# Kernel tuning notes

Hardware: AMD Instinct MI355X
Metric: run time of the kernel (lower is better)

Reference implementation:

```python
import jax, jax.numpy as jnp
import numpy as np

B, N, F, H, K = 4, 512, 64, 64, 64
EPS = 1e-14


def _pair_proj(h, W):
    # Linear over concat([h_j, h_i]) == h_j @ W[:F] + h_i @ W[F:], broadcast to [B,N,N,out]
    f = h.shape[-1]
    pj = h @ W[:f]   # [B,N,out] contribution of h.unsqueeze(-3) (index j)
    pi = h @ W[f:]   # [B,N,out] contribution of h.unsqueeze(-2) (index i)
    return pj[:, None, :, :] + pi[:, :, None, :]


def setup_inputs() -> dict:
    key = jax.random.key(0)
    ks = jax.random.split(key, 10)
    def w(k, shape, fan_in):
        return (jax.random.normal(k, shape, dtype=jnp.float32) / np.float32(np.sqrt(fan_in)))
    return {
        "h": jax.random.normal(ks[0], (B, N, F), dtype=jnp.float32),
        "x": jax.random.normal(ks[1], (B, N, 3), dtype=jnp.float32),
        "W_ew": w(ks[2], (2 * F, K), 2 * F), "b_ew": jnp.zeros((K,), jnp.float32),
        "W_sa": w(ks[3], (2 * F, 1), 2 * F),
        "W_es": w(ks[4], (2 * F + 1, H), 2 * F + 1), "b_es": jnp.zeros((H,), jnp.float32),
        "W_c1": w(ks[5], (H, H), H), "b_c1": jnp.zeros((H,), jnp.float32),
        "W_c2": w(ks[6], (H, 1), H), "b_c2": jnp.zeros((1,), jnp.float32),
        "W_n": w(ks[7], (F + H + K, H), F + H + K), "b_n": jnp.zeros((H,), jnp.float32),
    }


def reference(h, x, W_ew, b_ew, W_sa, W_es, b_es, W_c1, b_c1, W_c2, b_c2, W_n, b_n):
    # x_minus_xt[b,i,j] = x[b,j] - x[b,i]    [B,N,N,3]
    xmx = x[:, None, :, :] - x[:, :, None, :]
    norm = jnp.sqrt(jax.nn.relu(jnp.sum(xmx * xmx, axis=-1, keepdims=True)) + EPS)  # [B,N,N,1]
    spatial_att = jax.nn.softmax(norm, axis=-2)                                    # softmax over j
    filtered = 1.0 / (norm + 0.1)                                                  # [B,N,N,1]

    # edge_weight_mlp: tanh(Linear(2F -> K)) over h_cat_ht, without materializing the concat
    ew = jnp.tanh(_pair_proj(h, W_ew) + b_ew)                                      # [B,N,N,K]
    # semantic_attention_mlp: LeakyReLU(Linear(2F -> 1, no bias))
    sem_att = jax.nn.leaky_relu(_pair_proj(h, W_sa), negative_slope=0.01)          # [B,N,N,1]

    # x_minus_xt_att_sum = sum_j ew[b,i,j,k] * (xmx / norm^2)[b,i,j,c] -> [B,N,K,3]
    v = xmx / (norm * norm + EPS)
    att_sum = jnp.einsum('bijk,bijc->bikc', ew, v)
    att_norm = jnp.sqrt(jax.nn.relu(jnp.sum(att_sum * att_sum, axis=-1)) + EPS)    # [B,N,K]

    # edge_summary_mlp: SiLU(Linear(cat([filtered, h_j, h_i]) -> H))
    pre = filtered * W_es[0] + _pair_proj(h, W_es[1:]) + b_es                      # [B,N,N,H]
    h_e = jax.nn.silu(pre)

    # coordinate update: Linear->SiLU->Linear(H->1)
    coord = jax.nn.silu(h_e @ W_c1 + b_c1) @ W_c2 + b_c2                           # [B,N,N,1]
    x_new = jnp.sum(xmx * coord, axis=-2) + x                                      # sum over j

    h_e_agg = jnp.sum(sem_att * spatial_att * h_e, axis=-2)                        # [B,N,H]
    h_new = jnp.concatenate([h, h_e_agg, att_norm], axis=-1) @ W_n + b_n           # [B,N,H]
    return h_new, x_new
```

## Files before the change

kernel.cpp:

```cpp
#include <hip/hip_runtime.h>

#define B_ 4
#define N_ 512
#define F_ 64
#define H_ 64
#define K_ 64
#define BN_ (B_*N_)
#define EPS_ 1e-14f
#define TSC 2.8853900817779268f

typedef __attribute__((ext_vector_type(8))) short short8;
typedef __attribute__((ext_vector_type(4))) float f32x4;
typedef __attribute__((ext_vector_type(2))) float f32x2;

__device__ __forceinline__ unsigned short f2bf(float f) {
    const unsigned u = __float_as_uint(f);
    return (unsigned short)((u + 0x7FFFu + ((u >> 16) & 1u)) >> 16);
}
__device__ __forceinline__ unsigned short cvt_bf16(float f) {
    unsigned r;
    asm("v_cvt_pk_bf16_f32 %0, %1, %1" : "=v"(r) : "v"(f));
    return (unsigned short)r;
}
__device__ __forceinline__ unsigned cvt_pk_bf16(float lo, float hi) {
    unsigned r;
    asm("v_cvt_pk_bf16_f32 %0, %1, %2" : "=v"(r) : "v"(lo), "v"(hi));
    return r;
}
__device__ __forceinline__ float exp2_raw(float x) {
    float r;
    asm("v_exp_f32 %0, %1" : "=v"(r) : "v"(x));
    return r;
}
__device__ __forceinline__ float lane_bcast(float v, int lane) {
    return __int_as_float(__builtin_amdgcn_readlane(__float_as_int(v), lane));
}
__device__ __forceinline__ float rcpf(float x) { return __builtin_amdgcn_rcpf(x); }
__device__ __forceinline__ float fast_silu(float x) {
    return x * rcpf(1.0f + __expf(-x));
}

#define W_PJ2  0
#define W_PIEW (BN_*128)
#define W_PIES (BN_*128 + BN_*64)
#define W_PJSA (BN_*128 + 2*BN_*64)
#define W_PISA (BN_*128 + 2*BN_*64 + BN_)

__global__ __launch_bounds__(64) void proj_kernel(
    const float* __restrict__ h, const float* __restrict__ W_ew,
    const float* __restrict__ W_sa, const float* __restrict__ W_es,
    float* __restrict__ ws)
{
    const int node = blockIdx.x;
    const int t = threadIdx.x;
    __shared__ float sh[F_];
    sh[t] = h[node*F_ + t];
    __syncthreads();
    float a_jew=0.f, a_iew=0.f, a_jes=0.f, a_ies=0.f, a_jsa=0.f, a_isa=0.f;
    #pragma unroll 8
    for (int f = 0; f < F_; ++f) {
        const float hv = sh[f];
        a_jew += hv * W_ew[f*K_ + t];
        a_iew += hv * W_ew[(F_+f)*K_ + t];
        a_jes += hv * W_es[(1+f)*H_ + t];
        a_ies += hv * W_es[(1+F_+f)*H_ + t];
        a_jsa += hv * W_sa[f];
        a_isa += hv * W_sa[F_+f];
    }
    ws[W_PJ2 + (size_t)node*128 + t*2 + 0] = a_jew * TSC;
    ws[W_PJ2 + (size_t)node*128 + t*2 + 1] = a_jes;
    ws[W_PIEW + node*K_ + t] = a_iew;
    ws[W_PIES + node*H_ + t] = a_ies;
    if (t == 0) { ws[W_PJSA + node] = a_jsa; ws[W_PISA + node] = a_isa; }
}

__global__ __launch_bounds__(256, 6) void main_kernel(
    const float* __restrict__ h, const float* __restrict__ x,
    const float* __restrict__ b_ew, const float* __restrict__ b_es,
    const float* __restrict__ W_es, const float* __restrict__ W_c1,
    const float* __restrict__ b_c1, const float* __restrict__ W_c2,
    const float* __restrict__ b_c2, const float* __restrict__ W_n,
    const float* __restrict__ b_n,
    const float* __restrict__ ws, float* __restrict__ out)
{
    const int bi   = blockIdx.x;
    const int b    = bi >> 9;
    const int base = b * N_;
    const int tid  = threadIdx.x;
    const int w    = tid >> 6;
    const int lane = tid & 63;
    const int quad = lane >> 4;
    const int l16  = lane & 15;

    __shared__ unsigned short he_buf[4][16][72];
    __shared__ float sdA[4][64][4];
    __shared__ float coord_buf[4][64];
    __shared__ unsigned short WT[64*64];
    __shared__ float s_bw[64][2];

    float* const epi = (float*)&he_buf[0][0][0];
#define S_ATT(cmp, wv, ln) epi[(cmp)*256 + (wv)*64 + (ln)]
#define S_HEA(wv, ln)      epi[768 + (wv)*64 + (ln)]
#define S_MISC(wv, k)      epi[1024 + (wv)*4 + (k)]
#define S_CONCAT(m)        epi[1040 + (m)]
#define S_HNEW(wv, ln)     epi[1240 + (wv)*64 + (ln)]

    {
        const int col = tid & 63;
        const int k0  = (tid >> 6) * 16;
        const unsigned swz = (col & 7) << 4;
        #pragma unroll
        for (int m = 0; m < 8; ++m) {
            const int k = k0 + 2*m;
            const float f0 = W_c1[k*H_ + col];
            const float f1 = W_c1[(k+1)*H_ + col];
            *(unsigned*)((char*)WT + (col*128 + ((2*k) ^ swz))) = cvt_pk_bf16(f0, f1);
        }
        if (tid < 64) { s_bw[tid][0] = b_c1[tid]; s_bw[tid][1] = W_c2[tid]; }
    }

    const float pi_ew_t = (ws[W_PIEW + bi*K_ + lane] + b_ew[lane]) * TSC;
    const float pi_es_t = ws[W_PIES + bi*H_ + lane] + b_es[lane];
    const float pisa    = ws[W_PISA + bi];
    const float xi0 = x[bi*3+0], xi1 = x[bi*3+1], xi2 = x[bi*3+2];
    const float wes0_t = W_es[lane];
    const float bc2    = b_c2[0];

    const unsigned swzl = (l16 & 7) << 4;
    const unsigned offB0 = (unsigned)l16*128 + (((unsigned)quad*16) ^ swzl);
    const unsigned offB1 = (unsigned)l16*128 + ((64u + (unsigned)quad*16) ^ swzl);

    __syncthreads();

    float att0=0.f, att1=0.f, att2=0.f, hea=0.f, sume=0.f;
    float xa0=0.f, xa1=0.f, xa2=0.f;

    for (int c = 0; c < 2; ++c) {
        const int j0 = (w*2 + c) * 64;

        float esem, d0, d1, d2;
        {
            const int gj = base + j0 + lane;
            d0 = x[gj*3+0] - xi0;
            d1 = x[gj*3+1] - xi1;
            d2 = x[gj*3+2] - xi2;
            const float d2s = fmaf(d0,d0, fmaf(d1,d1, d2*d2));
            const float nrm = sqrtf(d2s + EPS_);
            const float e   = __expf(nrm);
            sume += e;
            const float filt = rcpf(nrm + 0.1f);
            const float inv  = rcpf(fmaf(nrm, nrm, EPS_));
            const float sv   = ws[W_PJSA + gj] + pisa;
            const float sem  = (sv >= 0.f) ? sv : 0.01f*sv;
            esem = e * sem;
            f32x4 p0 = { d0*inv, d1*inv, d2*inv, filt };
            *(f32x4*)&sdA[w][lane][0] = p0;
        }

        #pragma unroll
        for (int s = 0; s < 4; ++s) {
            const int sj = s*16;
            const float* pjp = ws + W_PJ2 + (size_t)(base + j0 + sj)*128 + lane*2;
            #pragma unroll 4
            for (int jj = 0; jj < 16; ++jj) {
                const f32x2 pj = *(const f32x2*)(pjp + (size_t)jj*128);
                const f32x4 p0 = *(const f32x4*)&sdA[w][sj + jj][0];
                const float esem_s = lane_bcast(esem, sj + jj);
                const float pre = fmaf(p0.w, wes0_t, pj.y + pi_es_t);
                const float he  = fast_silu(pre);
                hea = fmaf(esem_s, he, hea);
                he_buf[w][jj][lane] = cvt_bf16(he);
                const float ewt = fmaf(-2.0f, rcpf(exp2_raw(pj.x + pi_ew_t) + 1.0f), 1.0f);
                att0 = fmaf(ewt, p0.x, att0);
                att1 = fmaf(ewt, p0.y, att1);
                att2 = fmaf(ewt, p0.z, att2);
            }

            {
                const short8 a0 = *(const short8*)&he_buf[w][l16][quad*8];
                const short8 a1 = *(const short8*)&he_buf[w][l16][32 + quad*8];
                float rs0=0.f, rs1=0.f, rs2=0.f, rs3=0.f;
                #pragma unroll
                for (int nt = 0; nt < 4; ++nt) {
                    const short8 b0 = *(const short8*)((const char*)WT + (nt*2048 + offB0));
                    const short8 b1 = *(const short8*)((const char*)WT + (nt*2048 + offB1));
                    const f32x2 bw = *(const f32x2*)&s_bw[nt*16 + l16][0];
                    f32x4 acc = {0.f, 0.f, 0.f, 0.f};
                    acc = __builtin_amdgcn_mfma_f32_16x16x32_bf16(a0, b0, acc, 0, 0, 0);
                    acc = __builtin_amdgcn_mfma_f32_16x16x32_bf16(a1, b1, acc, 0, 0, 0);
                    rs0 += fast_silu(acc[0] + bw.x) * bw.y;
                    rs1 += fast_silu(acc[1] + bw.x) * bw.y;
                    rs2 += fast_silu(acc[2] + bw.x) * bw.y;
                    rs3 += fast_silu(acc[3] + bw.x) * bw.y;
                }
                #pragma unroll
                for (int m = 1; m <= 8; m <<= 1) {
                    rs0 += __shfl_xor(rs0, m, 64);
                    rs1 += __shfl_xor(rs1, m, 64);
                    rs2 += __shfl_xor(rs2, m, 64);
                    rs3 += __shfl_xor(rs3, m, 64);
                }
                if (l16 == 0) {
                    f32x4 cv = { rs0 + bc2, rs1 + bc2, rs2 + bc2, rs3 + bc2 };
                    *(f32x4*)&coord_buf[w][sj + quad*4] = cv;
                }
            }
        }

        {
            const float cj = coord_buf[w][lane];
            xa0 = fmaf(d0, cj, xa0);
            xa1 = fmaf(d1, cj, xa1);
            xa2 = fmaf(d2, cj, xa2);
        }
    }

    __syncthreads();

    #pragma unroll
    for (int m = 32; m >= 1; m >>= 1) {
        sume += __shfl_xor(sume, m, 64);
        xa0  += __shfl_xor(xa0,  m, 64);
        xa1  += __shfl_xor(xa1,  m, 64);
        xa2  += __shfl_xor(xa2,  m, 64);
    }
    S_ATT(0, w, lane) = att0;
    S_ATT(1, w, lane) = att1;
    S_ATT(2, w, lane) = att2;
    S_HEA(w, lane)    = hea;
    if (lane == 0) {
        S_MISC(w, 0) = sume; S_MISC(w, 1) = xa0; S_MISC(w, 2) = xa1; S_MISC(w, 3) = xa2;
    }
    __syncthreads();

    if (w == 0) {
        const float a0 = S_ATT(0,0,lane)+S_ATT(0,1,lane)+S_ATT(0,2,lane)+S_ATT(0,3,lane);
        const float a1 = S_ATT(1,0,lane)+S_ATT(1,1,lane)+S_ATT(1,2,lane)+S_ATT(1,3,lane);
        const float a2 = S_ATT(2,0,lane)+S_ATT(2,1,lane)+S_ATT(2,2,lane)+S_ATT(2,3,lane);
        const float hg = S_HEA(0,lane)+S_HEA(1,lane)+S_HEA(2,lane)+S_HEA(3,lane);
        const float se = S_MISC(0,0)+S_MISC(1,0)+S_MISC(2,0)+S_MISC(3,0);
        const float attn = sqrtf(fmaf(a0,a0, fmaf(a1,a1, a2*a2)) + EPS_);
        S_CONCAT(lane)       = h[bi*F_ + lane];
        S_CONCAT(64 + lane)  = hg * rcpf(se);
        S_CONCAT(128 + lane) = attn;
    }
    if (tid < 3) {
        const float xat = S_MISC(0,1+tid)+S_MISC(1,1+tid)+S_MISC(2,1+tid)+S_MISC(3,1+tid);
        out[(size_t)BN_*H_ + bi*3 + tid] = x[bi*3+tid] + xat;
    }
    __syncthreads();

    {
        float acc = 0.f;
        const int m0 = w * 48;
        #pragma unroll 8
        for (int m = m0; m < m0 + 48; ++m)
            acc = fmaf(S_CONCAT(m), W_n[m*H_ + lane], acc);
        S_HNEW(w, lane) = acc;
    }
    __syncthreads();
    if (w == 0) {
        out[bi*H_ + lane] = S_HNEW(0,lane) + S_HNEW(1,lane)
                          + S_HNEW(2,lane) + S_HNEW(3,lane) + b_n[lane];
    }
}

extern "C" void kernel_launch(void* const* d_in, const int* in_sizes, int n_in,
                              void* d_out, int out_size, void* d_ws, size_t ws_size,
                              hipStream_t stream) {
    (void)in_sizes; (void)n_in; (void)out_size; (void)ws_size;
    const float* h    = (const float*)d_in[0];
    const float* x    = (const float*)d_in[1];
    const float* W_ew = (const float*)d_in[2];
    const float* b_ew = (const float*)d_in[3];
    const float* W_sa = (const float*)d_in[4];
    const float* W_es = (const float*)d_in[5];
    const float* b_es = (const float*)d_in[6];
    const float* W_c1 = (const float*)d_in[7];
    const float* b_c1 = (const float*)d_in[8];
    const float* W_c2 = (const float*)d_in[9];
    const float* b_c2 = (const float*)d_in[10];
    const float* W_n  = (const float*)d_in[11];
    const float* b_n  = (const float*)d_in[12];
    float* out = (float*)d_out;
    float* ws  = (float*)d_ws;

    proj_kernel<<<dim3(BN_), dim3(64), 0, stream>>>(h, W_ew, W_sa, W_es, ws);
    main_kernel<<<dim3(BN_), dim3(256), 0, stream>>>(h, x, b_ew, b_es, W_es, W_c1,
                                                     b_c1, W_c2, b_c2, W_n, b_n, ws, out);
}
```

Baseline: 161.4 us.

## Batch 8 nodes per proj block with LDS-staged weights; relax main occupancy bound

```diff
diff --git a/kernel.cpp b/kernel.cpp
--- a/kernel.cpp
+++ b/kernel.cpp
@@ -46,35 +46,75 @@
 #define W_PJSA (BN_*128 + 2*BN_*64)
 #define W_PISA (BN_*128 + 2*BN_*64 + BN_)
 
-__global__ __launch_bounds__(64) void proj_kernel(
+__global__ __launch_bounds__(256) void proj_kernel(
     const float* __restrict__ h, const float* __restrict__ W_ew,
     const float* __restrict__ W_sa, const float* __restrict__ W_es,
     float* __restrict__ ws)
 {
-    const int node = blockIdx.x;
-    const int t = threadIdx.x;
-    __shared__ float sh[F_];
-    sh[t] = h[node*F_ + t];
-    __syncthreads();
-    float a_jew=0.f, a_iew=0.f, a_jes=0.f, a_ies=0.f, a_jsa=0.f, a_isa=0.f;
+    const int tid  = threadIdx.x;
+    const int w    = tid >> 6;
+    const int lane = tid & 63;
+    const int node0 = blockIdx.x * 8;
+
+    __shared__ float sW_ew[128][64];
+    __shared__ float sW_es[128][64];
+    __shared__ float sW_sa[128];
+    __shared__ float sh[8][64];
+
+    #pragma unroll
+    for (int it = 0; it < 32; ++it) {
+        const int idx = it*256 + tid;
+        sW_ew[idx>>6][idx&63] = W_ew[idx];
+        sW_es[idx>>6][idx&63] = W_es[64 + idx];
+    }
+    if (tid < 128) sW_sa[tid] = W_sa[tid];
+    #pragma unroll
+    for (int it = 0; it < 2; ++it) {
+        const int idx = it*256 + tid;
+        sh[idx>>6][idx&63] = h[node0*F_ + idx];
+    }
+    __syncthreads();
+
+    const int n0 = w*2;
+    float jew0=0.f,iew0=0.f,jes0=0.f,ies0=0.f;
+    float jew1=0.f,iew1=0.f,jes1=0.f,ies1=0.f;
     #pragma unroll 8
-    for (int f = 0; f < F_; ++f) {
-        const float hv = sh[f];
-        a_jew += hv * W_ew[f*K_ + t];
-        a_iew += hv * W_ew[(F_+f)*K_ + t];
-        a_jes += hv * W_es[(1+f)*H_ + t];
-        a_ies += hv * W_es[(1+F_+f)*H_ + t];
-        a_jsa += hv * W_sa[f];
-        a_isa += hv * W_sa[F_+f];
-    }
-    ws[W_PJ2 + (size_t)node*128 + t*2 + 0] = a_jew * TSC;
-    ws[W_PJ2 + (size_t)node*128 + t*2 + 1] = a_jes;
-    ws[W_PIEW + node*K_ + t] = a_iew;
-    ws[W_PIES + node*H_ + t] = a_ies;
-    if (t == 0) { ws[W_PJSA + node] = a_jsa; ws[W_PISA + node] = a_isa; }
-}
-
-__global__ __launch_bounds__(256, 6) void main_kernel(
+    for (int f = 0; f < 64; ++f) {
+        const float wje = sW_ew[f][lane],    wie = sW_ew[64+f][lane];
+        const float wjs = sW_es[f][lane],    wis = sW_es[64+f][lane];
+        const float h0  = sh[n0][f],         h1  = sh[n0+1][f];
+        jew0 = fmaf(h0, wje, jew0);  iew0 = fmaf(h0, wie, iew0);
+        jes0 = fmaf(h0, wjs, jes0);  ies0 = fmaf(h0, wis, ies0);
+        jew1 = fmaf(h1, wje, jew1);  iew1 = fmaf(h1, wie, iew1);
+        jes1 = fmaf(h1, wjs, jes1);  ies1 = fmaf(h1, wis, ies1);
+    }
+    float p0 = sh[n0][lane]   * sW_sa[lane];
+    float q0 = sh[n0][lane]   * sW_sa[64+lane];
+    float p1 = sh[n0+1][lane] * sW_sa[lane];
+    float q1 = sh[n0+1][lane] * sW_sa[64+lane];
+    #pragma unroll
+    for (int m = 32; m >= 1; m >>= 1) {
+        p0 += __shfl_xor(p0, m, 64);  q0 += __shfl_xor(q0, m, 64);
+        p1 += __shfl_xor(p1, m, 64);  q1 += __shfl_xor(q1, m, 64);
+    }
+
+    const int g0 = node0 + n0;
+    const int g1 = g0 + 1;
+    ws[W_PJ2 + (size_t)g0*128 + lane*2 + 0] = jew0 * TSC;
+    ws[W_PJ2 + (size_t)g0*128 + lane*2 + 1] = jes0;
+    ws[W_PJ2 + (size_t)g1*128 + lane*2 + 0] = jew1 * TSC;
+    ws[W_PJ2 + (size_t)g1*128 + lane*2 + 1] = jes1;
+    ws[W_PIEW + g0*K_ + lane] = iew0;
+    ws[W_PIEW + g1*K_ + lane] = iew1;
+    ws[W_PIES + g0*H_ + lane] = ies0;
+    ws[W_PIES + g1*H_ + lane] = ies1;
+    if (lane == 0) {
+        ws[W_PJSA + g0] = p0;  ws[W_PISA + g0] = q0;
+        ws[W_PJSA + g1] = p1;  ws[W_PISA + g1] = q1;
+    }
+}
+
+__global__ __launch_bounds__(256, 5) void main_kernel(
     const float* __restrict__ h, const float* __restrict__ x,
     const float* __restrict__ b_ew, const float* __restrict__ b_es,
     const float* __restrict__ W_es, const float* __restrict__ W_c1,
@@ -285,7 +325,7 @@
     float* out = (float*)d_out;
     float* ws  = (float*)d_ws;
 
-    proj_kernel<<<dim3(BN_), dim3(64), 0, stream>>>(h, W_ew, W_sa, W_es, ws);
+    proj_kernel<<<dim3(BN_/8), dim3(256), 0, stream>>>(h, W_ew, W_sa, W_es, ws);
     main_kernel<<<dim3(BN_), dim3(256), 0, stream>>>(h, x, b_ew, b_es, W_es, W_c1,
                                                      b_c1, W_c2, b_c2, W_n, b_n, ws, out);
 }
```

New measurement: 156.6 us. 1.03x faster.
